# Kernel tuning notes

Measured on AMD Instinct MI355X. Metric: run time of the kernel, lower is better.

The kernel has to match this reference:

```python
import jax, jax.numpy as jnp
import numpy as np

B, S, D = 4, 2048, 1024
H, DH = 16, 64


def setup_inputs() -> dict:
    key = jax.random.key(0)
    ks = jax.random.split(key, 5)
    x = jax.random.normal(ks[0], (B, S, D), dtype=jnp.float32)
    # causal mask: True where attention is disallowed (j > i)
    mask = jnp.triu(jnp.ones((S, S), dtype=bool), k=1)
    mask = jnp.broadcast_to(mask, (B, S, S))
    scale = 1.0 / np.sqrt(D)
    w_q = jax.random.normal(ks[1], (D, D), dtype=jnp.float32) * scale
    w_k = jax.random.normal(ks[2], (D, D), dtype=jnp.float32) * scale
    w_v = jax.random.normal(ks[3], (D, D), dtype=jnp.float32) * scale
    w_o = jax.random.normal(ks[4], (D, D), dtype=jnp.float32) * scale
    return {"x": x, "mask": mask, "w_q": w_q, "w_k": w_k, "w_v": w_v, "w_o": w_o}


def reference(x, mask, w_q, w_k, w_v, w_o):
    # torch Linear: y = x @ W.T (bias=False)
    b, s, d = x.shape
    q = (x @ w_q.T).reshape(b, s, H, DH).transpose(0, 2, 1, 3)  # [B,H,S,DH]
    k = (x @ w_k.T).reshape(b, s, H, DH).transpose(0, 2, 1, 3)
    v = (x @ w_v.T).reshape(b, s, H, DH).transpose(0, 2, 1, 3)
    inv_sqrt_dh = jnp.asarray(1.0 / np.sqrt(DH), dtype=x.dtype)
    scores = jnp.einsum('bhqd,bhkd->bhqk', q * inv_sqrt_dh, k)  # [B,H,S,S]
    scores = jnp.where(mask[:, None, :, :], -jnp.inf, scores)
    attn = jax.nn.softmax(scores, axis=-1)  # dropout is identity in eval mode
    out = jnp.einsum('bhqk,bhkd->bhqd', attn, v)  # [B,H,S,DH]
    out = out.transpose(0, 2, 1, 3).reshape(b, s, d)
    out = out @ w_o.T
    return out, attn
```

## Files before the change

### kernel.cpp

```cpp
#include <hip/hip_runtime.h>

#define DEV __device__ __forceinline__

typedef __attribute__((ext_vector_type(8))) short short8;
typedef __attribute__((ext_vector_type(4))) float f32x4;

DEV unsigned short f2bf(float f) {
  unsigned u = __builtin_bit_cast(unsigned, f);
  u += 0x7fff + ((u >> 16) & 1);
  return (unsigned short)(u >> 16);
}

DEV void gload_lds16(const void* g, void* l) {
  __builtin_amdgcn_global_load_lds(
      (const __attribute__((address_space(1))) void*)g,
      (__attribute__((address_space(3))) void*)l, 16, 0, 0);
}

#if __has_builtin(__builtin_amdgcn_exp2f)
#define EXP2F(x) __builtin_amdgcn_exp2f(x)
#else
#define EXP2F(x) exp2f(x)
#endif

#define LOG2E 1.4426950408889634f
#define QSCALE (0.125f * LOG2E)
#define MFMA16(a, b, c) __builtin_amdgcn_mfma_f32_16x16x32_bf16((a), (b), (c), 0, 0, 0)

__global__ void cvt_f32_bf16(const float* __restrict__ in, unsigned short* __restrict__ out, int n4) {
  int i = blockIdx.x * blockDim.x + threadIdx.x;
  int stride = gridDim.x * blockDim.x;
  for (; i < n4; i += stride) {
    float4 v = ((const float4*)in)[i];
    ushort4 o;
    o.x = f2bf(v.x); o.y = f2bf(v.y); o.z = f2bf(v.z); o.w = f2bf(v.w);
    ((ushort4*)out)[i] = o;
  }
}

#define GK 1024
template <int MODE>
__global__ __launch_bounds__(256) void gemm_bt(const unsigned short* __restrict__ A,
                                               const unsigned short* __restrict__ Bw,
                                               void* __restrict__ Cout) {
  __shared__ unsigned short Ash[128 * 32];
  __shared__ unsigned short Bsh[128 * 32];
  const int tid = threadIdx.x;
  const int lane = tid & 63;
  const int w = tid >> 6;
  const int wm = w >> 1, wn = w & 1;
  const int l15 = lane & 15, l4 = lane >> 4;
  const int row0 = blockIdx.y * 128;
  const int col0 = blockIdx.x * 128;

  f32x4 acc[4][4] = {};

  for (int kt = 0; kt < GK; kt += 32) {
    __syncthreads();
#pragma unroll
    for (int c = 0; c < 2; ++c) {
      int o = c * 4096 + tid * 16;
      int ldsoff = c * 4096 + w * 1024;
      int row = o >> 6, colb = o & 63;
      gload_lds16((const char*)A + (size_t)(row0 + row) * 2048 + kt * 2 + colb,
                  (char*)Ash + ldsoff);
      gload_lds16((const char*)Bw + (size_t)(col0 + row) * 2048 + kt * 2 + colb,
                  (char*)Bsh + ldsoff);
    }
    __syncthreads();
    short8 af[4], bf[4];
#pragma unroll
    for (int m = 0; m < 4; ++m)
      af[m] = *(const short8*)((const char*)Ash + (wm * 64 + m * 16 + l15) * 64 + l4 * 16);
#pragma unroll
    for (int n = 0; n < 4; ++n)
      bf[n] = *(const short8*)((const char*)Bsh + (wn * 64 + n * 16 + l15) * 64 + l4 * 16);
#pragma unroll
    for (int m = 0; m < 4; ++m)
#pragma unroll
      for (int n = 0; n < 4; ++n)
        acc[m][n] = MFMA16(af[m], bf[n], acc[m][n]);
  }

#pragma unroll
  for (int m = 0; m < 4; ++m)
#pragma unroll
    for (int n = 0; n < 4; ++n)
#pragma unroll
      for (int r = 0; r < 4; ++r) {
        int mrow = row0 + wm * 64 + m * 16 + l4 * 4 + r;
        int ncol = col0 + wn * 64 + n * 16 + l15;
        float v = acc[m][n][r];
        if (MODE == 0) {
          ((unsigned short*)Cout)[(size_t)mrow * 1024 + ncol] = f2bf(v);
        } else if (MODE == 1) {
          int b = mrow >> 11, s = mrow & 2047, h = ncol >> 6, d = ncol & 63;
          ((unsigned short*)Cout)[((size_t)((b * 16 + h) * 64 + d)) * 2048 + s] = f2bf(v);
        } else if (MODE == 2) {
          ((float*)Cout)[(size_t)mrow * 1024 + ncol] = v;
        } else {
          ((unsigned short*)Cout)[(size_t)mrow * 1024 + ncol] = f2bf(v * QSCALE);
        }
      }
}


DEV void stage_tile(const unsigned short* src_base, size_t row_stride, int col0,
                    char* ldsbase, int tid) {
  const int w = tid >> 6;
  const int r0 = tid >> 3;
  const int c0 = (tid & 7) ^ (r0 & 7);
  gload_lds16((const char*)(src_base + (size_t)r0 * row_stride + col0 + c0 * 8),
              ldsbase + w * 1024);
  const int r1 = 32 + r0;
  gload_lds16((const char*)(src_base + (size_t)r1 * row_stride + col0 + c0 * 8),
              ldsbase + 4096 + w * 1024);
}

__global__ __launch_bounds__(256, 4) void attn_fused(const unsigned short* __restrict__ Q,
                                                     const unsigned short* __restrict__ Kb,
                                                     const unsigned short* __restrict__ Vt,
                                                     float* __restrict__ attn,
                                                     unsigned short* __restrict__ O) {
  __shared__ char lds[40960];

  const int tid = threadIdx.x, lane = tid & 63, w = tid >> 6;
  const int l15 = lane & 15, l4 = lane >> 4;
  const int s7 = l15 & 7;
  const int off0 = (l4 ^ s7) << 4;
  const int off1 = ((l4 + 4) ^ s7) << 4;
  const int pr = blockIdx.x;
  const int bh = blockIdx.y;
  const int b = bh >> 4, h = bh & 15;

  const size_t qk_base = ((size_t)b * 2048) * 1024 + h * 64;
  const unsigned short* Qp = Q + qk_base;
  const unsigned short* Kp = Kb + qk_base;
  const unsigned short* Vp = Vt + (size_t)bh * 64 * 2048;
  float* Ap = attn + (size_t)bh * 2048 * 2048;
  char* pbase = lds + 32768 + w * 2048;

  for (int t = 0; t < 2; ++t) {
    const int qt = t ? (31 - pr) : pr;
    const int q0 = qt * 64 + w * 16;
    const int myq = q0 + l15;

    short8 qf[2];
    {
      const char* qrow = (const char*)(Qp + (size_t)(q0 + l15) * 1024);
      qf[0] = *(const short8*)(qrow + (l4 * 8) * 2);
      qf[1] = *(const short8*)(qrow + (32 + l4 * 8) * 2);
    }

    float lacc[4] = {0.f, 0.f, 0.f, 0.f};
    stage_tile(Kp, 1024, 0, lds, tid);
    __syncthreads();
    for (int jt = 0; jt <= qt; ++jt) {
      const char* kb = lds + (jt & 1) * 8192;
      if (jt < qt) stage_tile(Kp + (size_t)(jt + 1) * 64 * 1024, 1024, 0,
                              lds + ((jt + 1) & 1) * 8192, tid);
      const int jbase = jt * 64;
      const bool diag = (jt == qt);
#pragma unroll
      for (int jb = 0; jb < 4; ++jb) {
        const char* krow = kb + (jb * 16 + l15) * 128;
        short8 k0 = *(const short8*)(krow + off0);
        short8 k1 = *(const short8*)(krow + off1);
        f32x4 a = {};
        a = MFMA16(k0, qf[0], a);
        a = MFMA16(k1, qf[1], a);
#pragma unroll
        for (int r = 0; r < 4; ++r) {
          int j = jbase + jb * 16 + l4 * 4 + r;
          float e = EXP2F(a[r]);
          lacc[r] += (diag && j > myq) ? 0.f : e;
        }
      }
      __syncthreads();
    }
    float lsum = (lacc[0] + lacc[1]) + (lacc[2] + lacc[3]);
    lsum += __shfl_xor(lsum, 16);
    lsum += __shfl_xor(lsum, 32);
    const float inv_l = 1.f / lsum;

    f32x4 oacc[4] = {};
    stage_tile(Kp, 1024, 0, lds, tid);
    stage_tile(Vp, 2048, 0, lds + 16384, tid);
    __syncthreads();
    for (int jt = 0; jt <= qt; ++jt) {
      const char* kb = lds + (jt & 1) * 8192;
      const char* vb = lds + 16384 + (jt & 1) * 8192;
      if (jt < qt) {
        stage_tile(Kp + (size_t)(jt + 1) * 64 * 1024, 1024, 0,
                   lds + ((jt + 1) & 1) * 8192, tid);
        stage_tile(Vp, 2048, (jt + 1) * 64, lds + 16384 + ((jt + 1) & 1) * 8192, tid);
      }
      const int jbase = jt * 64;
      const bool diag = (jt == qt);
      float p[16];
#pragma unroll
      for (int jb = 0; jb < 4; ++jb) {
        const char* krow = kb + (jb * 16 + l15) * 128;
        short8 k0 = *(const short8*)(krow + off0);
        short8 k1 = *(const short8*)(krow + off1);
        f32x4 a = {};
        a = MFMA16(k0, qf[0], a);
        a = MFMA16(k1, qf[1], a);
#pragma unroll
        for (int r = 0; r < 4; ++r) {
          int j = jbase + jb * 16 + l4 * 4 + r;
          float e = EXP2F(a[r]) * inv_l;
          p[jb * 4 + r] = (diag && j > myq) ? 0.f : e;
        }
      }
#pragma unroll
      for (int jb = 0; jb < 4; ++jb) {
        f32x4 pv = {p[jb * 4], p[jb * 4 + 1], p[jb * 4 + 2], p[jb * 4 + 3]};
        *(f32x4*)(Ap + (size_t)myq * 2048 + jbase + jb * 16 + l4 * 4) = pv;
      }
#pragma unroll
      for (int jb = 0; jb < 4; ++jb) {
        unsigned u0 = f2bf(p[jb * 4]) | ((unsigned)f2bf(p[jb * 4 + 1]) << 16);
        unsigned u1 = f2bf(p[jb * 4 + 2]) | ((unsigned)f2bf(p[jb * 4 + 3]) << 16);
        uint2 uu; uu.x = u0; uu.y = u1;
        *(uint2*)(pbase + (jb * 2 + (l4 >> 1)) * 256 + l15 * 16 + (l4 & 1) * 8) = uu;
      }
      short8 pa0 = *(const short8*)(pbase + l4 * 256 + l15 * 16);
      short8 pa1 = *(const short8*)(pbase + (4 + l4) * 256 + l15 * 16);
#pragma unroll
      for (int db = 0; db < 4; ++db) {
        const char* vrow = vb + (db * 16 + l15) * 128;
        short8 v0 = *(const short8*)(vrow + off0);
        short8 v1 = *(const short8*)(vrow + off1);
        oacc[db] = MFMA16(pa0, v0, oacc[db]);
        oacc[db] = MFMA16(pa1, v1, oacc[db]);
      }
      __syncthreads();
    }

    for (int jt = qt + 1; jt < 32; ++jt) {
      const int jbase = jt * 64;
      f32x4 z = {};
#pragma unroll
      for (int jb = 0; jb < 4; ++jb)
        *(f32x4*)(Ap + (size_t)myq * 2048 + jbase + jb * 16 + l4 * 4) = z;
    }

#pragma unroll
    for (int db = 0; db < 4; ++db)
#pragma unroll
      for (int r = 0; r < 4; ++r) {
        int q = q0 + l4 * 4 + r;
        int d = db * 16 + l15;
        O[((size_t)b * 2048 + q) * 1024 + h * 64 + d] = f2bf(oacc[db][r]);
      }
  }
}

extern "C" void kernel_launch(void* const* d_in, const int* in_sizes, int n_in,
                              void* d_out, int out_size, void* d_ws, size_t ws_size,
                              hipStream_t stream) {
  const float* x  = (const float*)d_in[0];
  const float* wq = (const float*)d_in[2];
  const float* wk = (const float*)d_in[3];
  const float* wv = (const float*)d_in[4];
  const float* wo = (const float*)d_in[5];

  float* out  = (float*)d_out;
  float* attn = out + (size_t)8192 * 1024;

  char* ws = (char*)d_ws;
  const size_t MB = 1 << 20;
  unsigned short* xb  = (unsigned short*)(ws);
  unsigned short* wqb = (unsigned short*)(ws + 16 * MB);
  unsigned short* wkb = (unsigned short*)(ws + 18 * MB);
  unsigned short* wvb = (unsigned short*)(ws + 20 * MB);
  unsigned short* wob = (unsigned short*)(ws + 22 * MB);
  unsigned short* Qb  = (unsigned short*)(ws + 24 * MB);
  unsigned short* Kb  = (unsigned short*)(ws + 40 * MB);
  unsigned short* Vtb = (unsigned short*)(ws + 56 * MB);
  unsigned short* Ob  = (unsigned short*)(ws + 72 * MB);

  cvt_f32_bf16<<<2048, 256, 0, stream>>>(x, xb, 8192 * 1024 / 4);
  cvt_f32_bf16<<<1024, 256, 0, stream>>>(wq, wqb, 1024 * 1024 / 4);
  cvt_f32_bf16<<<1024, 256, 0, stream>>>(wk, wkb, 1024 * 1024 / 4);
  cvt_f32_bf16<<<1024, 256, 0, stream>>>(wv, wvb, 1024 * 1024 / 4);
  cvt_f32_bf16<<<1024, 256, 0, stream>>>(wo, wob, 1024 * 1024 / 4);

  dim3 ggrid(8, 64);
  gemm_bt<3><<<ggrid, 256, 0, stream>>>(xb, wqb, Qb);
  gemm_bt<0><<<ggrid, 256, 0, stream>>>(xb, wkb, Kb);
  gemm_bt<1><<<ggrid, 256, 0, stream>>>(xb, wvb, Vtb);

  attn_fused<<<dim3(16, 64), 256, 0, stream>>>(Qb, Kb, Vtb, attn, Ob);

  gemm_bt<2><<<ggrid, 256, 0, stream>>>(Ob, wob, out);
}
```

Measured before the change: 487.2 us.

## Merge weight casts and QKV GEMMs, remap attention blocks per XCD, pair K tiles

The four weight conversions become one kernel launch, and the three QKV projection GEMMs become one launch with a z-dimension selecting the weight and output layout. This cuts launch count and lets the GEMMs fill the device together. The attention grid is flattened and remapped so blocks sharing a (batch, head) land on the same XCD, which is meant to improve L2 reuse of K and V. The softmax-denominator pass now stages two K tiles per barrier, which uses more LDS per stage and needs fewer syncs.

```diff
diff --git a/kernel.cpp b/kernel.cpp
--- a/kernel.cpp
+++ b/kernel.cpp
@@ -38,11 +38,24 @@
   }
 }
 
+__global__ void cvt_w4(const float* __restrict__ w0, const float* __restrict__ w1,
+                       const float* __restrict__ w2, const float* __restrict__ w3,
+                       unsigned short* __restrict__ o0, unsigned short* __restrict__ o1,
+                       unsigned short* __restrict__ o2, unsigned short* __restrict__ o3) {
+  int i = blockIdx.x * blockDim.x + threadIdx.x;
+  int sel = i >> 18, j = i & 0x3ffff;
+  const float* in = sel == 0 ? w0 : sel == 1 ? w1 : sel == 2 ? w2 : w3;
+  unsigned short* out = sel == 0 ? o0 : sel == 1 ? o1 : sel == 2 ? o2 : o3;
+  float4 v = ((const float4*)in)[j];
+  ushort4 o;
+  o.x = f2bf(v.x); o.y = f2bf(v.y); o.z = f2bf(v.z); o.w = f2bf(v.w);
+  ((ushort4*)out)[j] = o;
+}
+
 #define GK 1024
 template <int MODE>
-__global__ __launch_bounds__(256) void gemm_bt(const unsigned short* __restrict__ A,
-                                               const unsigned short* __restrict__ Bw,
-                                               void* __restrict__ Cout) {
+DEV void gemm_body(const unsigned short* A, const unsigned short* Bw, void* Cout,
+                   int bx, int by) {
   __shared__ unsigned short Ash[128 * 32];
   __shared__ unsigned short Bsh[128 * 32];
   const int tid = threadIdx.x;
@@ -50,8 +63,8 @@
   const int w = tid >> 6;
   const int wm = w >> 1, wn = w & 1;
   const int l15 = lane & 15, l4 = lane >> 4;
-  const int row0 = blockIdx.y * 128;
-  const int col0 = blockIdx.x * 128;
+  const int row0 = by * 128;
+  const int col0 = bx * 128;
 
   f32x4 acc[4][4] = {};
 
@@ -104,6 +117,25 @@
       }
 }
 
+__global__ __launch_bounds__(256) void gemm_qkv(const unsigned short* __restrict__ A,
+                                                const unsigned short* __restrict__ Wq,
+                                                const unsigned short* __restrict__ Wk,
+                                                const unsigned short* __restrict__ Wv,
+                                                unsigned short* __restrict__ Qo,
+                                                unsigned short* __restrict__ Ko,
+                                                unsigned short* __restrict__ Vto) {
+  const int z = blockIdx.z;
+  if (z == 0)      gemm_body<3>(A, Wq, Qo,  blockIdx.x, blockIdx.y);
+  else if (z == 1) gemm_body<0>(A, Wk, Ko,  blockIdx.x, blockIdx.y);
+  else             gemm_body<1>(A, Wv, Vto, blockIdx.x, blockIdx.y);
+}
+
+__global__ __launch_bounds__(256) void gemm_out(const unsigned short* __restrict__ A,
+                                                const unsigned short* __restrict__ Bw,
+                                                float* __restrict__ Cout) {
+  gemm_body<2>(A, Bw, Cout, blockIdx.x, blockIdx.y);
+}
+
 
 DEV void stage_tile(const unsigned short* src_base, size_t row_stride, int col0,
                     char* ldsbase, int tid) {
@@ -129,8 +161,10 @@
   const int s7 = l15 & 7;
   const int off0 = (l4 ^ s7) << 4;
   const int off1 = ((l4 + 4) ^ s7) << 4;
-  const int pr = blockIdx.x;
-  const int bh = blockIdx.y;
+  const int F = blockIdx.x;
+  const int xcd = F & 7, slot = F >> 3;
+  const int pr = slot & 15;
+  const int bh = xcd + ((slot >> 4) << 3);
   const int b = bh >> 4, h = bh & 15;
 
   const size_t qk_base = ((size_t)b * 2048) * 1024 + h * 64;
@@ -153,30 +187,45 @@
     }
 
     float lacc[4] = {0.f, 0.f, 0.f, 0.f};
-    stage_tile(Kp, 1024, 0, lds, tid);
-    __syncthreads();
-    for (int jt = 0; jt <= qt; ++jt) {
-      const char* kb = lds + (jt & 1) * 8192;
-      if (jt < qt) stage_tile(Kp + (size_t)(jt + 1) * 64 * 1024, 1024, 0,
-                              lds + ((jt + 1) & 1) * 8192, tid);
-      const int jbase = jt * 64;
-      const bool diag = (jt == qt);
-#pragma unroll
-      for (int jb = 0; jb < 4; ++jb) {
-        const char* krow = kb + (jb * 16 + l15) * 128;
-        short8 k0 = *(const short8*)(krow + off0);
-        short8 k1 = *(const short8*)(krow + off1);
-        f32x4 a = {};
-        a = MFMA16(k0, qf[0], a);
-        a = MFMA16(k1, qf[1], a);
-#pragma unroll
-        for (int r = 0; r < 4; ++r) {
-          int j = jbase + jb * 16 + l4 * 4 + r;
-          float e = EXP2F(a[r]);
-          lacc[r] += (diag && j > myq) ? 0.f : e;
+    {
+      stage_tile(Kp, 1024, 0, lds, tid);
+      if (qt >= 1) stage_tile(Kp + (size_t)64 * 1024, 1024, 0, lds + 8192, tid);
+      __syncthreads();
+      const int nst = (qt + 2) >> 1;
+      for (int st = 0; st < nst; ++st) {
+        char* kbb = lds + (st & 1) * 16384;
+        const int jt0 = 2 * st;
+        if (jt0 + 2 <= qt) {
+          char* nb = lds + ((st + 1) & 1) * 16384;
+          stage_tile(Kp + (size_t)(jt0 + 2) * 64 * 1024, 1024, 0, nb, tid);
+          if (jt0 + 3 <= qt)
+            stage_tile(Kp + (size_t)(jt0 + 3) * 64 * 1024, 1024, 0, nb + 8192, tid);
         }
-      }
-      __syncthreads();
+#pragma unroll
+        for (int u = 0; u < 2; ++u) {
+          const int jt = jt0 + u;
+          if (jt > qt) break;
+          const char* kb = kbb + u * 8192;
+          const int jbase = jt * 64;
+          const bool diag = (jt == qt);
+#pragma unroll
+          for (int jb = 0; jb < 4; ++jb) {
+            const char* krow = kb + (jb * 16 + l15) * 128;
+            short8 k0 = *(const short8*)(krow + off0);
+            short8 k1 = *(const short8*)(krow + off1);
+            f32x4 a = {};
+            a = MFMA16(k0, qf[0], a);
+            a = MFMA16(k1, qf[1], a);
+#pragma unroll
+            for (int r = 0; r < 4; ++r) {
+              int j = jbase + jb * 16 + l4 * 4 + r;
+              float e = EXP2F(a[r]);
+              lacc[r] += (diag && j > myq) ? 0.f : e;
+            }
+          }
+        }
+        __syncthreads();
+      }
     }
     float lsum = (lacc[0] + lacc[1]) + (lacc[2] + lacc[3]);
     lsum += __shfl_xor(lsum, 16);
@@ -282,17 +331,11 @@
   unsigned short* Ob  = (unsigned short*)(ws + 72 * MB);
 
   cvt_f32_bf16<<<2048, 256, 0, stream>>>(x, xb, 8192 * 1024 / 4);
-  cvt_f32_bf16<<<1024, 256, 0, stream>>>(wq, wqb, 1024 * 1024 / 4);
-  cvt_f32_bf16<<<1024, 256, 0, stream>>>(wk, wkb, 1024 * 1024 / 4);
-  cvt_f32_bf16<<<1024, 256, 0, stream>>>(wv, wvb, 1024 * 1024 / 4);
-  cvt_f32_bf16<<<1024, 256, 0, stream>>>(wo, wob, 1024 * 1024 / 4);
-
-  dim3 ggrid(8, 64);
-  gemm_bt<3><<<ggrid, 256, 0, stream>>>(xb, wqb, Qb);
-  gemm_bt<0><<<ggrid, 256, 0, stream>>>(xb, wkb, Kb);
-  gemm_bt<1><<<ggrid, 256, 0, stream>>>(xb, wvb, Vtb);
-
-  attn_fused<<<dim3(16, 64), 256, 0, stream>>>(Qb, Kb, Vtb, attn, Ob);
-
-  gemm_bt<2><<<ggrid, 256, 0, stream>>>(Ob, wob, out);
-}
+  cvt_w4<<<4096, 256, 0, stream>>>(wq, wk, wv, wo, wqb, wkb, wvb, wob);
+
+  gemm_qkv<<<dim3(8, 64, 3), 256, 0, stream>>>(xb, wqb, wkb, wvb, Qb, Kb, Vtb);
+
+  attn_fused<<<1024, 256, 0, stream>>>(Qb, Kb, Vtb, attn, Ob);
+
+  gemm_out<<<dim3(8, 64), 256, 0, stream>>>(Ob, wob, out);
+}
```

Result: faster. 446.7 us (-8.3%).
